# Kernel optimization log

Measured on AMD Instinct MI355X. Metric: run time of the kernel, lower is better.

The kernel has to match this reference:

```python
import jax, jax.numpy as jnp
import numpy as np

INF = 1000000000000.0
B, H, EMB = 64, 512, 512
V = 32000
S_ENC, S_SEQ = 512, 512
ENC2 = 512  # 2 * encoder_hidden_dim
NUM_OOV = 50


def setup_inputs() -> dict:
    key = jax.random.key(0)
    ks = jax.random.split(key, 24)
    s = 0.02
    nrm = lambda k, shp: jax.random.normal(k, shp, jnp.float32) * s
    inp = {}
    inp["input_ids"] = jax.random.randint(ks[0], (B,), 0, V)
    inp["prev_context"] = jax.random.normal(ks[1], (B, H), jnp.float32)
    inp["h0"] = jax.random.normal(ks[2], (1, B, H), jnp.float32)
    inp["c0"] = jax.random.normal(ks[3], (1, B, H), jnp.float32)
    inp["encoder_outputs"] = jax.random.normal(ks[4], (B, S_ENC, H), jnp.float32)
    inp["seqs_encoding"] = jax.random.normal(ks[5], (B, S_SEQ, ENC2), jnp.float32)
    inp["seqs_encoding_mask"] = jax.random.randint(ks[6], (B, S_SEQ), 0, 2).astype(bool)
    ext = jax.random.randint(ks[7], (B, S_SEQ), 0, V + NUM_OOV)
    inp["ext_idx"] = ext.at[0, 0].set(V + NUM_OOV - 1)  # pin max so num_oov=NUM_OOV
    # parameters (torch Linear convention: y = x @ W.T + b)
    inp["embed"] = nrm(ks[8], (V, EMB))
    inp["W_reduce"] = nrm(ks[9], (EMB, EMB + H)); inp["b_reduce"] = jnp.zeros((EMB,), jnp.float32)
    inp["W_key"] = nrm(ks[10], (H, H)); inp["b_key"] = jnp.zeros((H,), jnp.float32)
    inp["W_comb"] = nrm(ks[11], (H, 2 * H)); inp["b_comb"] = jnp.zeros((H,), jnp.float32)
    inp["W_seqkey"] = nrm(ks[12], (H, ENC2))
    inp["W_ih"] = nrm(ks[13], (4 * H, EMB)); inp["W_hh"] = nrm(ks[14], (4 * H, H))
    inp["b_ih"] = jnp.zeros((4 * H,), jnp.float32); inp["b_hh"] = jnp.zeros((4 * H,), jnp.float32)
    inp["W_out"] = nrm(ks[15], (V, H)); inp["b_out"] = jnp.zeros((V,), jnp.float32)
    return inp


def reference(input_ids, prev_context, h0, c0, encoder_outputs, seqs_encoding,
              seqs_encoding_mask, ext_idx, embed, W_reduce, b_reduce, W_key, b_key,
              W_comb, b_comb, W_seqkey, W_ih, W_hh, b_ih, b_hh, W_out, b_out):
    # embed + (dropout is identity at p=0 / eval) + reduce
    embedded = embed[input_ids]                                   # [B, EMB]
    x = jnp.concatenate([embedded, prev_context], axis=1) @ W_reduce.T + b_reduce  # [B, EMB]
    # single-step, single-layer LSTM (PyTorch gate order i, f, g, o)
    h, c = h0[0], c0[0]
    gates = x @ W_ih.T + b_ih + h @ W_hh.T + b_hh                 # [B, 4H]
    i, f, g, o = jnp.split(gates, 4, axis=-1)
    c1 = jax.nn.sigmoid(f) * c + jax.nn.sigmoid(i) * jnp.tanh(g)
    h1 = jax.nn.sigmoid(o) * jnp.tanh(c1)                         # [B, H]
    output = h1
    # masked attention over encoder_outputs
    enc_mask = encoder_outputs.sum(axis=-1) == 0                  # [B, S_enc]
    keys = encoder_outputs @ W_key.T + b_key                      # [B, S_enc, H]
    energies = jnp.einsum('bsh,bh->bs', keys, output)
    energies = jnp.where(enc_mask, 1e-12, energies)
    attn_weights = jax.nn.softmax(energies, axis=-1)
    context = jnp.einsum('bs,bsh->bh', attn_weights, encoder_outputs)  # [B, H]
    combined = jnp.tanh(jnp.concatenate([output, context], axis=1) @ W_comb.T + b_comb)
    logits = combined @ W_out.T + b_out                           # [B, V]
    # masked attention energies over token sequence for the copy mechanism
    seq_keys = jnp.tanh(seqs_encoding @ W_seqkey.T)               # [B, S_seq, H]
    seq_energies = jnp.einsum('bsh,bh->bs', seq_keys, output)
    seq_energies = jnp.where(seqs_encoding_mask, 1e-12, seq_energies)
    # extended vocab + scatter_max pointer-copy
    extended = jnp.concatenate([logits, jnp.zeros((B, NUM_OOV), logits.dtype)], axis=1)  # [B, V+OOV]
    copy = jnp.full_like(extended, -INF)
    copy = copy.at[jnp.arange(B)[:, None], ext_idx].max(seq_energies)
    copy = jnp.where(copy == -INF, 0.0, copy)
    out = extended + copy
    out = jnp.where(out == 0.0, -INF, out)
    out = jax.nn.log_softmax(out, axis=1)
    return (out, context, h1[None], c1[None], attn_weights)
```

## Files before the change

kernel.cpp:

```cpp
#include <hip/hip_runtime.h>
#include <math.h>

#define B_N    64
#define H_N    512
#define V_N    32000
#define S_N    512
#define VEXT   32050
#define INF_F  1000000000000.0f

typedef __attribute__((ext_vector_type(4))) float floatx4;
typedef __attribute__((ext_vector_type(8))) __bf16 bf16x8;

#define OFF_OUT0 0
#define OFF_CTX  (B_N * VEXT)
#define OFF_H1   (OFF_CTX + B_N * H_N)
#define OFF_C1   (OFF_H1 + B_N * H_N)
#define OFF_ATTN (OFF_C1 + B_N * H_N)

#define WS_FLAG   0
#define WS_X      16
#define WS_GATES  (WS_X + B_N * H_N)
#define WS_Q      (WS_GATES + B_N * 4 * H_N)
#define WS_KB     (WS_Q + B_N * H_N)
#define WS_EN     (WS_KB + B_N)
#define WS_COMB   (WS_EN + B_N * S_N)
#define WS_SEQE   (WS_COMB + B_N * H_N)
#define WS_WSKBF  (WS_SEQE + B_N * S_N)
#define WS_LOGITS (WS_WSKBF + (H_N * H_N) / 2)
#define WS_COPY   (WS_LOGITS + B_N * V_N)
#define WS_RMAX   (WS_COPY + B_N * VEXT)
#define WS_RSUM   (WS_RMAX + B_N)

__device__ __forceinline__ float sigm(float x) { return 1.0f / (1.0f + expf(-x)); }

__device__ __forceinline__ unsigned short f2bf(float f) {
    unsigned u = __float_as_uint(f);
    u += 0x7fffu + ((u >> 16) & 1u);
    return (unsigned short)(u >> 16);
}
__device__ __forceinline__ float bf2f(unsigned short h) {
    return __uint_as_float(((unsigned)h) << 16);
}

__device__ __forceinline__ unsigned enc_f(float f) {
    unsigned u = __float_as_uint(f);
    return (u & 0x80000000u) ? ~u : (u | 0x80000000u);
}
__device__ __forceinline__ float dec_f(unsigned e) {
    unsigned u = (e & 0x80000000u) ? (e & 0x7fffffffu) : ~e;
    return __uint_as_float(u);
}

__global__ void kDetect(const unsigned int* __restrict__ m, int* __restrict__ flag) {
    __shared__ int any;
    if (threadIdx.x == 0) any = 0;
    __syncthreads();
    int loc = 0;
    for (int i = threadIdx.x; i < 8192; i += 256) loc |= (m[i] > 1u) ? 1 : 0;
    if (loc) any = 1;
    __syncthreads();
    if (threadIdx.x == 0) *flag = any;
}

__global__ void kConvertW(const float* __restrict__ W, unsigned short* __restrict__ swzh,
                          unsigned short* __restrict__ swzl) {
    const int g = blockIdx.x * 256 + threadIdx.x;
    const int t = g >> 10, kc = (g >> 6) & 15, lane = g & 63;
    const int r = t * 16 + (lane & 15);
    const int k = kc * 32 + (lane >> 4) * 8;
    const float* src = W + (size_t)r * 512 + k;
    ushort4 h0, h1, l0, l1;
    {
        const float4 v0 = *(const float4*)(src);
        const float4 v1 = *(const float4*)(src + 4);
        h0.x = f2bf(v0.x); l0.x = f2bf(v0.x - bf2f(h0.x));
        h0.y = f2bf(v0.y); l0.y = f2bf(v0.y - bf2f(h0.y));
        h0.z = f2bf(v0.z); l0.z = f2bf(v0.z - bf2f(h0.z));
        h0.w = f2bf(v0.w); l0.w = f2bf(v0.w - bf2f(h0.w));
        h1.x = f2bf(v1.x); l1.x = f2bf(v1.x - bf2f(h1.x));
        h1.y = f2bf(v1.y); l1.y = f2bf(v1.y - bf2f(h1.y));
        h1.z = f2bf(v1.z); l1.z = f2bf(v1.z - bf2f(h1.z));
        h1.w = f2bf(v1.w); l1.w = f2bf(v1.w - bf2f(h1.w));
    }
    *(ushort4*)(swzh + (size_t)g * 8) = h0;
    *(ushort4*)(swzh + (size_t)g * 8 + 4) = h1;
    *(ushort4*)(swzl + (size_t)g * 8) = l0;
    *(ushort4*)(swzl + (size_t)g * 8 + 4) = l1;
}

__global__ void kFillCopy(unsigned int* __restrict__ copyenc,
                          unsigned int* __restrict__ rmax, float* __restrict__ rsum) {
    const unsigned NE = enc_f(-INF_F);
    if (blockIdx.x == 0 && threadIdx.x < B_N) {
        rmax[threadIdx.x] = 0u;
        rsum[threadIdx.x] = 0.0f;
    }
    int i0 = (blockIdx.x * 256 + threadIdx.x) * 4;
#pragma unroll
    for (int k = 0; k < 4; k++) {
        int i = i0 + k;
        if (i < B_N * VEXT) copyenc[i] = NE;
    }
}

__global__ __launch_bounds__(256) void kEmbedReduce(
        const int* __restrict__ ids, const float* __restrict__ embed,
        const float* __restrict__ pctx, const float* __restrict__ Wred,
        const float* __restrict__ bred, float* __restrict__ x) {
    __shared__ float xc[1024];
    const int tid = threadIdx.x;
    const int b = blockIdx.x >> 1, half = blockIdx.x & 1;
    const float* er = embed + (size_t)ids[b] * 512;
    xc[tid] = er[tid];               xc[tid + 256] = er[tid + 256];
    xc[512 + tid] = pctx[b * 512 + tid]; xc[512 + tid + 256] = pctx[b * 512 + tid + 256];
    __syncthreads();
    const int j = half * 256 + tid;
    const float4* w4 = (const float4*)(Wred + (size_t)j * 1024);
    const float4* x4 = (const float4*)xc;
    float acc = bred[j];
    for (int k = 0; k < 256; k++) {
        float4 w = w4[k], xv = x4[k];
        acc += w.x * xv.x + w.y * xv.y + w.z * xv.z + w.w * xv.w;
    }
    x[b * 512 + j] = acc;
}

__global__ __launch_bounds__(256) void kGates(
        const float* __restrict__ x, const float* __restrict__ h0,
        const float* __restrict__ Wih, const float* __restrict__ Whh,
        const float* __restrict__ bih, const float* __restrict__ bhh,
        float* __restrict__ gates) {
    __shared__ float xl[512], hl[512];
    const int tid = threadIdx.x;
    const int b = blockIdx.x >> 3, part = blockIdx.x & 7;
    xl[tid] = x[b * 512 + tid];  xl[tid + 256] = x[b * 512 + tid + 256];
    hl[tid] = h0[b * 512 + tid]; hl[tid + 256] = h0[b * 512 + tid + 256];
    __syncthreads();
    const int j = part * 256 + tid;
    const float4* wi4 = (const float4*)(Wih + (size_t)j * 512);
    const float4* wh4 = (const float4*)(Whh + (size_t)j * 512);
    const float4* x4 = (const float4*)xl;
    const float4* h4 = (const float4*)hl;
    float acc = bih[j] + bhh[j];
    for (int k = 0; k < 128; k++) {
        float4 w = wi4[k], xv = x4[k];
        acc += w.x * xv.x + w.y * xv.y + w.z * xv.z + w.w * xv.w;
    }
    for (int k = 0; k < 128; k++) {
        float4 w = wh4[k], hv = h4[k];
        acc += w.x * hv.x + w.y * hv.y + w.z * hv.z + w.w * hv.w;
    }
    gates[(size_t)b * 2048 + j] = acc;
}

__global__ __launch_bounds__(256) void kLstm(
        const float* __restrict__ gates, const float* __restrict__ c0,
        float* __restrict__ h1o, float* __restrict__ c1o) {
    const int idx = blockIdx.x * 256 + threadIdx.x;
    const int b = idx >> 9, j = idx & 511;
    const float gi = gates[(size_t)b * 2048 + j];
    const float gf = gates[(size_t)b * 2048 + 512 + j];
    const float gg = gates[(size_t)b * 2048 + 1024 + j];
    const float go = gates[(size_t)b * 2048 + 1536 + j];
    const float cp = c0[idx];
    const float c1 = sigm(gf) * cp + sigm(gi) * tanhf(gg);
    const float h1 = sigm(go) * tanhf(c1);
    h1o[idx] = h1;
    c1o[idx] = c1;
}

__global__ __launch_bounds__(256) void kQ(
        const float* __restrict__ h1, const float* __restrict__ Wkey,
        const float* __restrict__ bkey, float* __restrict__ q, float* __restrict__ kb) {
    __shared__ float hl[512];
    __shared__ float rd[256];
    const int tid = threadIdx.x;
    const int b = blockIdx.x >> 1, half = blockIdx.x & 1;
    hl[tid] = h1[b * 512 + tid]; hl[tid + 256] = h1[b * 512 + tid + 256];
    __syncthreads();
    const int k = half * 256 + tid;
    float acc = 0.f;
#pragma unroll 4
    for (int h = 0; h < 512; h++) acc += hl[h] * Wkey[(size_t)h * 512 + k];
    q[b * 512 + k] = acc;
    if (half == 0) {
        float p = bkey[tid] * hl[tid] + bkey[tid + 256] * hl[tid + 256];
        rd[tid] = p; __syncthreads();
        for (int st = 128; st > 0; st >>= 1) {
            if (tid < st) rd[tid] += rd[tid + st];
            __syncthreads();
        }
        if (tid == 0) kb[b] = rd[0];
    }
}

__global__ __launch_bounds__(256) void kEnergies(
        const float* __restrict__ enc, const float* __restrict__ q,
        const float* __restrict__ kb, float* __restrict__ energ) {
    __shared__ float ql[512];
    __shared__ float pe[256], ps[256];
    const int tid = threadIdx.x;
    const int b = blockIdx.x >> 2;
    const int sc = (blockIdx.x & 3) * 128;
    ql[tid] = q[b * 512 + tid]; ql[tid + 256] = q[b * 512 + tid + 256];
    __syncthreads();
    const int r = tid & 127, hi = tid >> 7;
    const float4* row4 = (const float4*)(enc + (size_t)(b * 512 + sc + r) * 512 + hi * 256);
    const float4* q4 = (const float4*)(ql + hi * 256);
    float e = 0.f, ssum = 0.f;
#pragma unroll 4
    for (int k = 0; k < 64; k++) {
        float4 ev = row4[k], qv = q4[k];
        e += ev.x * qv.x + ev.y * qv.y + ev.z * qv.z + ev.w * qv.w;
        ssum += ev.x + ev.y + ev.z + ev.w;
    }
    pe[tid] = e; ps[tid] = ssum;
    __syncthreads();
    if (tid < 128) {
        float ee = pe[tid] + pe[tid + 128] + kb[b];
        float sm = ps[tid] + ps[tid + 128];
        if (sm == 0.0f) ee = 1e-12f;
        energ[b * 512 + sc + tid] = ee;
    }
}

__global__ __launch_bounds__(256) void kSoftmax(
        const float* __restrict__ energ, float* __restrict__ attn) {
    __shared__ float el[512];
    __shared__ float rd[256];
    const int tid = threadIdx.x, b = blockIdx.x;
    el[tid] = energ[b * 512 + tid]; el[tid + 256] = energ[b * 512 + tid + 256];
    __syncthreads();
    rd[tid] = fmaxf(el[tid], el[tid + 256]); __syncthreads();
    for (int st = 128; st > 0; st >>= 1) {
        if (tid < st) rd[tid] = fmaxf(rd[tid], rd[tid + st]);
        __syncthreads();
    }
    const float m = rd[0]; __syncthreads();
    float v0 = expf(el[tid] - m), v1 = expf(el[tid + 256] - m);
    rd[tid] = v0 + v1; __syncthreads();
    for (int st = 128; st > 0; st >>= 1) {
        if (tid < st) rd[tid] += rd[tid + st];
        __syncthreads();
    }
    const float inv = 1.0f / rd[0];
    attn[b * 512 + tid] = v0 * inv;
    attn[b * 512 + tid + 256] = v1 * inv;
}

__global__ __launch_bounds__(256) void kContext(
        const float* __restrict__ enc, const float* __restrict__ attn,
        float* __restrict__ ctx) {
    __shared__ float al[64];
    const int tid = threadIdx.x;
    const int b = blockIdx.x >> 3, sc = (blockIdx.x & 7) * 64;
    if (tid < 64) al[tid] = attn[b * 512 + sc + tid];
    __syncthreads();
    float a0 = 0.f, a1 = 0.f;
    for (int s = 0; s < 64; s++) {
        const float* row = enc + (size_t)(b * 512 + sc + s) * 512;
        const float av = al[s];
        a0 += av * row[tid];
        a1 += av * row[tid + 256];
    }
    atomicAdd(&ctx[b * 512 + tid], a0);
    atomicAdd(&ctx[b * 512 + tid + 256], a1);
}

__global__ __launch_bounds__(256) void kCombined(
        const float* __restrict__ h1, const float* __restrict__ ctx,
        const float* __restrict__ Wcomb, const float* __restrict__ bcomb,
        float* __restrict__ comb) {
    __shared__ float hc[1024];
    const int tid = threadIdx.x;
    const int b = blockIdx.x >> 1, half = blockIdx.x & 1;
    hc[tid] = h1[b * 512 + tid];        hc[tid + 256] = h1[b * 512 + tid + 256];
    hc[512 + tid] = ctx[b * 512 + tid]; hc[512 + tid + 256] = ctx[b * 512 + tid + 256];
    __syncthreads();
    const int j = half * 256 + tid;
    const float4* w4 = (const float4*)(Wcomb + (size_t)j * 1024);
    const float4* x4 = (const float4*)hc;
    float acc = bcomb[j];
    for (int k = 0; k < 256; k++) {
        float4 w = w4[k], xv = x4[k];
        acc += w.x * xv.x + w.y * xv.y + w.z * xv.z + w.w * xv.w;
    }
    comb[b * 512 + j] = tanhf(acc);
}

__global__ __launch_bounds__(256) void kLogits(
        const float* __restrict__ comb, const float* __restrict__ Wout,
        const float* __restrict__ bout, float* __restrict__ logits) {
    __shared__ float cl[4][32][64];
    const int tid = threadIdx.x;
    const int vt = tid & 63, kq = tid >> 6;
    const int v = blockIdx.x * 64 + vt;
    float acc[64];
#pragma unroll
    for (int i = 0; i < 64; i++) acc[i] = 0.f;
    for (int kc = 0; kc < 4; kc++) {
        __syncthreads();
        {
            const float4* s4 = (const float4*)(comb + (size_t)vt * 512 + kq * 128 + kc * 32);
#pragma unroll
            for (int qq = 0; qq < 8; qq++) {
                float4 vv = s4[qq];
                cl[kq][qq * 4 + 0][vt] = vv.x; cl[kq][qq * 4 + 1][vt] = vv.y;
                cl[kq][qq * 4 + 2][vt] = vv.z; cl[kq][qq * 4 + 3][vt] = vv.w;
            }
        }
        __syncthreads();
        float wreg[32];
        const float4* w4 = (const float4*)(Wout + (size_t)v * 512 + kq * 128 + kc * 32);
#pragma unroll
        for (int qq = 0; qq < 8; qq++) {
            float4 wv = w4[qq];
            wreg[qq * 4 + 0] = wv.x; wreg[qq * 4 + 1] = wv.y;
            wreg[qq * 4 + 2] = wv.z; wreg[qq * 4 + 3] = wv.w;
        }
#pragma unroll
        for (int kk = 0; kk < 32; kk++) {
            const float wv = wreg[kk];
            const float4* cp = (const float4*)&cl[kq][kk][0];
#pragma unroll
            for (int b4 = 0; b4 < 16; b4++) {
                float4 c4 = cp[b4];
                acc[b4 * 4 + 0] += wv * c4.x; acc[b4 * 4 + 1] += wv * c4.y;
                acc[b4 * 4 + 2] += wv * c4.z; acc[b4 * 4 + 3] += wv * c4.w;
            }
        }
    }
    float* red = &cl[0][0][0];
    __syncthreads();
    if (kq >= 2) {
#pragma unroll
        for (int b = 0; b < 64; b++) red[(kq - 2) * 4096 + vt * 64 + b] = acc[b];
    }
    __syncthreads();
    if (kq < 2) {
#pragma unroll
        for (int b = 0; b < 64; b++) acc[b] += red[kq * 4096 + vt * 64 + b];
    }
    __syncthreads();
    if (kq == 1) {
#pragma unroll
        for (int b = 0; b < 64; b++) red[vt * 64 + b] = acc[b];
    }
    __syncthreads();
    if (kq == 0) {
        const float bo = bout[v];
#pragma unroll
        for (int b = 0; b < 64; b++)
            logits[(size_t)b * 32000 + v] = acc[b] + red[vt * 64 + b] + bo;
    }
}

#define A_STRIDE 520
#define MT 32
__global__ __launch_bounds__(512, 4) void kSeqGemm(
        const float* __restrict__ seqs, const unsigned short* __restrict__ swzh,
        const unsigned short* __restrict__ swzl,
        const float* __restrict__ h1g, float* __restrict__ seq_e) {
    __shared__ unsigned short a_hi[MT * A_STRIDE];
    __shared__ unsigned short a_lo[MT * A_STRIDE];
    __shared__ float h1l[512];
    __shared__ float partf[8][MT];
    const int tid = threadIdx.x;
    const int m0 = blockIdx.x * MT;
    const int b = blockIdx.x >> 4;
    const int w = tid >> 6;
    const int lane = tid & 63;
    const int quad = lane >> 4;
    const int c16 = lane & 15;

    h1l[tid] = h1g[b * 512 + tid];

    {
        const int row = tid >> 4, seg = tid & 15;
        const float* src = seqs + (size_t)(m0 + row) * 512 + seg * 4;
        unsigned short* dh = &a_hi[row * A_STRIDE + seg * 4];
        unsigned short* dl = &a_lo[row * A_STRIDE + seg * 4];
#pragma unroll
        for (int i = 0; i < 8; i++) {
            float4 v = *(const float4*)(src + i * 64);
            ushort4 hv, lv;
            hv.x = f2bf(v.x); lv.x = f2bf(v.x - bf2f(hv.x));
            hv.y = f2bf(v.y); lv.y = f2bf(v.y - bf2f(hv.y));
            hv.z = f2bf(v.z); lv.z = f2bf(v.z - bf2f(hv.z));
            hv.w = f2bf(v.w); lv.w = f2bf(v.w - bf2f(hv.w));
            *(ushort4*)(dh + i * 64) = hv;
            *(ushort4*)(dl + i * 64) = lv;
        }
    }
    __syncthreads();

    floatx4 acc[2][4];
    const floatx4 zf = {0.f, 0.f, 0.f, 0.f};
#pragma unroll
    for (int i = 0; i < 2; i++)
#pragma unroll
        for (int j = 0; j < 4; j++) acc[i][j] = zf;

    const size_t boff = (size_t)((w * 4) * 16) * 512 + (size_t)lane * 8;
    const unsigned short* bh = swzh + boff;
    const unsigned short* bl = swzl + boff;
#pragma unroll 2
    for (int kc = 0; kc < 16; kc++) {
        bf16x8 ah[2], al[2], bhf[4], blf[4];
#pragma unroll
        for (int nt = 0; nt < 4; nt++) {
            bhf[nt] = *(const bf16x8*)(bh + (size_t)(nt * 16 + kc) * 512);
            blf[nt] = *(const bf16x8*)(bl + (size_t)(nt * 16 + kc) * 512);
        }
#pragma unroll
        for (int ms = 0; ms < 2; ms++) {
            ah[ms] = *(const bf16x8*)&a_hi[(ms * 16 + c16) * A_STRIDE + kc * 32 + quad * 8];
            al[ms] = *(const bf16x8*)&a_lo[(ms * 16 + c16) * A_STRIDE + kc * 32 + quad * 8];
        }
#pragma unroll
        for (int ms = 0; ms < 2; ms++)
#pragma unroll
            for (int nt = 0; nt < 4; nt++) {
                acc[ms][nt] = __builtin_amdgcn_mfma_f32_16x16x32_bf16(
                    ah[ms], bhf[nt], acc[ms][nt], 0, 0, 0);
                acc[ms][nt] = __builtin_amdgcn_mfma_f32_16x16x32_bf16(
                    al[ms], bhf[nt], acc[ms][nt], 0, 0, 0);
                acc[ms][nt] = __builtin_amdgcn_mfma_f32_16x16x32_bf16(
                    ah[ms], blf[nt], acc[ms][nt], 0, 0, 0);
            }
    }

    float psum[8];
#pragma unroll
    for (int i = 0; i < 8; i++) psum[i] = 0.f;
#pragma unroll
    for (int ms = 0; ms < 2; ms++)
#pragma unroll
        for (int nt = 0; nt < 4; nt++) {
            const float hv = h1l[w * 64 + nt * 16 + c16];
#pragma unroll
            for (int r = 0; r < 4; r++)
                psum[ms * 4 + r] += tanhf(acc[ms][nt][r]) * hv;
        }
#pragma unroll
    for (int d = 1; d < 16; d <<= 1)
#pragma unroll
        for (int i = 0; i < 8; i++) psum[i] += __shfl_xor(psum[i], d);
    if (c16 == 0) {
#pragma unroll
        for (int ms = 0; ms < 2; ms++)
#pragma unroll
            for (int r = 0; r < 4; r++)
                partf[w][ms * 16 + quad * 4 + r] = psum[ms * 4 + r];
    }
    __syncthreads();
    if (tid < MT) {
        float s = 0.f;
#pragma unroll
        for (int ww = 0; ww < 8; ww++) s += partf[ww][tid];
        seq_e[m0 + tid] = s;
    }
}

__global__ __launch_bounds__(512) void kScatter(
        const float* __restrict__ seq_e, const void* __restrict__ mask,
        const int* __restrict__ extix, const int* __restrict__ flag,
        unsigned int* __restrict__ copyenc) {
    const int tid = threadIdx.x, b = blockIdx.x;
    float e = seq_e[b * 512 + tid];
    bool mk;
    if (*flag) mk = ((const unsigned char*)mask)[b * 512 + tid] != 0;
    else       mk = ((const int*)mask)[b * 512 + tid] != 0;
    if (mk) e = 1e-12f;
    const int idx = extix[b * 512 + tid];
    atomicMax(&copyenc[(size_t)b * VEXT + idx], enc_f(e));
}

__global__ __launch_bounds__(256) void kFinal1(
        const float* __restrict__ logits, const unsigned int* __restrict__ copyenc,
        float* __restrict__ out0, unsigned int* __restrict__ rmax) {
    __shared__ float rd[4];
    const int tid = threadIdx.x;
    const int b = blockIdx.x >> 4, chunk = blockIdx.x & 15;
    const int base = chunk * 2048 + tid;
    const float* lrow = logits + (size_t)b * 32000;
    const unsigned int* crow = copyenc + (size_t)b * VEXT;
    float* orow = out0 + (size_t)b * VEXT;
    float lm = -3.0e38f;
#pragma unroll
    for (int k = 0; k < 8; k++) {
        const int j = base + k * 256;
        if (j < VEXT) {
            float ext = (j < 32000) ? lrow[j] : 0.0f;
            float cv = dec_f(crow[j]);
            if (cv == -INF_F) cv = 0.0f;
            float o = ext + cv;
            if (o == 0.0f) o = -INF_F;
            orow[j] = o;
            lm = fmaxf(lm, o);
        }
    }
#pragma unroll
    for (int d = 1; d < 64; d <<= 1) lm = fmaxf(lm, __shfl_xor(lm, d));
    if ((tid & 63) == 0) rd[tid >> 6] = lm;
    __syncthreads();
    if (tid == 0) {
        float m = fmaxf(fmaxf(rd[0], rd[1]), fmaxf(rd[2], rd[3]));
        atomicMax(&rmax[b], enc_f(m));
    }
}

__global__ __launch_bounds__(256) void kFinal2(
        const float* __restrict__ out0, const unsigned int* __restrict__ rmax,
        float* __restrict__ rsum) {
    __shared__ float rd[4];
    const int tid = threadIdx.x;
    const int b = blockIdx.x >> 4, chunk = blockIdx.x & 15;
    const int base = chunk * 2048 + tid;
    const float* orow = out0 + (size_t)b * VEXT;
    const float m = dec_f(rmax[b]);
    float s = 0.f;
#pragma unroll
    for (int k = 0; k < 8; k++) {
        const int j = base + k * 256;
        if (j < VEXT) s += expf(orow[j] - m);
    }
#pragma unroll
    for (int d = 1; d < 64; d <<= 1) s += __shfl_xor(s, d);
    if ((tid & 63) == 0) rd[tid >> 6] = s;
    __syncthreads();
    if (tid == 0) atomicAdd(&rsum[b], rd[0] + rd[1] + rd[2] + rd[3]);
}

__global__ __launch_bounds__(256) void kFinal3(
        float* __restrict__ out0, const unsigned int* __restrict__ rmax,
        const float* __restrict__ rsum) {
    const int tid = threadIdx.x;
    const int b = blockIdx.x >> 4, chunk = blockIdx.x & 15;
    const int base = chunk * 2048 + tid;
    float* orow = out0 + (size_t)b * VEXT;
    const float lse = dec_f(rmax[b]) + logf(rsum[b]);
#pragma unroll
    for (int k = 0; k < 8; k++) {
        const int j = base + k * 256;
        if (j < VEXT) orow[j] -= lse;
    }
}

extern "C" void kernel_launch(void* const* d_in, const int* in_sizes, int n_in,
                              void* d_out, int out_size, void* d_ws, size_t ws_size,
                              hipStream_t stream) {
    const int*   ids   = (const int*)d_in[0];
    const float* pctx  = (const float*)d_in[1];
    const float* h0    = (const float*)d_in[2];
    const float* c0    = (const float*)d_in[3];
    const float* enc   = (const float*)d_in[4];
    const float* seqs  = (const float*)d_in[5];
    const void*  mask  = d_in[6];
    const int*   extix = (const int*)d_in[7];
    const float* embed = (const float*)d_in[8];
    const float* Wred  = (const float*)d_in[9];
    const float* bred  = (const float*)d_in[10];
    const float* Wkey  = (const float*)d_in[11];
    const float* bkey  = (const float*)d_in[12];
    const float* Wcomb = (const float*)d_in[13];
    const float* bcomb = (const float*)d_in[14];
    const float* Wseqk = (const float*)d_in[15];
    const float* Wih   = (const float*)d_in[16];
    const float* Whh   = (const float*)d_in[17];
    const float* bih   = (const float*)d_in[18];
    const float* bhh   = (const float*)d_in[19];
    const float* Wout  = (const float*)d_in[20];
    const float* bout  = (const float*)d_in[21];
    (void)in_sizes; (void)n_in; (void)out_size; (void)ws_size;

    float* out = (float*)d_out;
    float* ws = (float*)d_ws;
    int* flag = (int*)ws;
    float* xws = ws + WS_X;
    float* gatesws = ws + WS_GATES;
    float* qws = ws + WS_Q;
    float* kbws = ws + WS_KB;
    float* enws = ws + WS_EN;
    float* combws = ws + WS_COMB;
    float* seqews = ws + WS_SEQE;
    unsigned short* wskh = (unsigned short*)(ws + WS_WSKBF);
    float* logitsws = ws + WS_LOGITS;
    unsigned short* wskl = (unsigned short*)(ws + WS_LOGITS);
    unsigned int* copyenc = (unsigned int*)(ws + WS_COPY);
    unsigned int* rmax = (unsigned int*)(ws + WS_RMAX);
    float* rsum = ws + WS_RSUM;

    kDetect<<<1, 256, 0, stream>>>((const unsigned int*)mask, flag);
    kConvertW<<<128, 256, 0, stream>>>(Wseqk, wskh, wskl);
    kFillCopy<<<2004, 256, 0, stream>>>(copyenc, rmax, rsum);
    kEmbedReduce<<<128, 256, 0, stream>>>(ids, embed, pctx, Wred, bred, xws);
    kGates<<<512, 256, 0, stream>>>(xws, h0, Wih, Whh, bih, bhh, gatesws);
    kLstm<<<128, 256, 0, stream>>>(gatesws, c0, out + OFF_H1, out + OFF_C1);
    kSeqGemm<<<1024, 512, 0, stream>>>(seqs, wskh, wskl, out + OFF_H1, seqews);
    kScatter<<<64, 512, 0, stream>>>(seqews, mask, extix, flag, copyenc);
    kQ<<<128, 256, 0, stream>>>(out + OFF_H1, Wkey, bkey, qws, kbws);
    kEnergies<<<256, 256, 0, stream>>>(enc, qws, kbws, enws);
    kSoftmax<<<64, 256, 0, stream>>>(enws, out + OFF_ATTN);
    hipMemsetAsync(out + OFF_CTX, 0, (size_t)B_N * H_N * sizeof(float), stream);
    kContext<<<512, 256, 0, stream>>>(enc, out + OFF_ATTN, out + OFF_CTX);
    kCombined<<<128, 256, 0, stream>>>(out + OFF_H1, out + OFF_CTX, Wcomb, bcomb, combws);
    kLogits<<<500, 256, 0, stream>>>(combws, Wout, bout, logitsws);
    kFinal1<<<1024, 256, 0, stream>>>(logitsws, copyenc, out + OFF_OUT0, rmax);
    kFinal2<<<1024, 256, 0, stream>>>(out + OFF_OUT0, rmax, rsum);
    kFinal3<<<1024, 256, 0, stream>>>(out + OFF_OUT0, rmax, rsum);
}
```

Measured before the change: 592.3 us.

## Enlarge seq-key GEMM tile to 128 rows with K-chunking and fuse scatter-max

The seq-key GEMM block tile grows from 32 to 128 rows. The A operand is staged through shared memory in four K-chunks of 128, so each W_seqkey fragment loaded from global memory is reused across 8 M-subtiles instead of 2. This cuts B-operand traffic and the block count from 1024 to 256, at the cost of many more accumulator registers (occupancy hint drops to 2) and extra barriers per chunk. The separate scatter kernel is folded into the GEMM epilogue, which removes one launch and the seq_e round trip through global memory.

```diff
diff --git a/kernel.cpp b/kernel.cpp
--- a/kernel.cpp
+++ b/kernel.cpp
@@ -355,19 +355,19 @@
     }
 }
 
-#define A_STRIDE 520
-#define MT 32
-__global__ __launch_bounds__(512, 4) void kSeqGemm(
+#define ACH 136
+__global__ __launch_bounds__(512, 2) void kSeqGemm(
         const float* __restrict__ seqs, const unsigned short* __restrict__ swzh,
-        const unsigned short* __restrict__ swzl,
-        const float* __restrict__ h1g, float* __restrict__ seq_e) {
-    __shared__ unsigned short a_hi[MT * A_STRIDE];
-    __shared__ unsigned short a_lo[MT * A_STRIDE];
+        const unsigned short* __restrict__ swzl, const float* __restrict__ h1g,
+        const void* __restrict__ mask, const int* __restrict__ extix,
+        const int* __restrict__ flag, unsigned int* __restrict__ copyenc) {
+    __shared__ unsigned short a_hi[128 * ACH];
+    __shared__ unsigned short a_lo[128 * ACH];
     __shared__ float h1l[512];
-    __shared__ float partf[8][MT];
-    const int tid = threadIdx.x;
-    const int m0 = blockIdx.x * MT;
-    const int b = blockIdx.x >> 4;
+    __shared__ float partf[8][128];
+    const int tid = threadIdx.x;
+    const int m0 = blockIdx.x * 128;
+    const int b = blockIdx.x >> 2;
     const int w = tid >> 6;
     const int lane = tid & 63;
     const int quad = lane >> 4;
@@ -375,66 +375,69 @@
 
     h1l[tid] = h1g[b * 512 + tid];
 
-    {
-        const int row = tid >> 4, seg = tid & 15;
-        const float* src = seqs + (size_t)(m0 + row) * 512 + seg * 4;
-        unsigned short* dh = &a_hi[row * A_STRIDE + seg * 4];
-        unsigned short* dl = &a_lo[row * A_STRIDE + seg * 4];
-#pragma unroll
-        for (int i = 0; i < 8; i++) {
-            float4 v = *(const float4*)(src + i * 64);
-            ushort4 hv, lv;
-            hv.x = f2bf(v.x); lv.x = f2bf(v.x - bf2f(hv.x));
-            hv.y = f2bf(v.y); lv.y = f2bf(v.y - bf2f(hv.y));
-            hv.z = f2bf(v.z); lv.z = f2bf(v.z - bf2f(hv.z));
-            hv.w = f2bf(v.w); lv.w = f2bf(v.w - bf2f(hv.w));
-            *(ushort4*)(dh + i * 64) = hv;
-            *(ushort4*)(dl + i * 64) = lv;
-        }
-    }
-    __syncthreads();
-
-    floatx4 acc[2][4];
+    floatx4 acc[8][4];
     const floatx4 zf = {0.f, 0.f, 0.f, 0.f};
 #pragma unroll
-    for (int i = 0; i < 2; i++)
+    for (int i = 0; i < 8; i++)
 #pragma unroll
         for (int j = 0; j < 4; j++) acc[i][j] = zf;
 
-    const size_t boff = (size_t)((w * 4) * 16) * 512 + (size_t)lane * 8;
+    const size_t boff = (size_t)(w * 64) * 512 + (size_t)lane * 8;
     const unsigned short* bh = swzh + boff;
     const unsigned short* bl = swzl + boff;
-#pragma unroll 2
-    for (int kc = 0; kc < 16; kc++) {
-        bf16x8 ah[2], al[2], bhf[4], blf[4];
-#pragma unroll
-        for (int nt = 0; nt < 4; nt++) {
-            bhf[nt] = *(const bf16x8*)(bh + (size_t)(nt * 16 + kc) * 512);
-            blf[nt] = *(const bf16x8*)(bl + (size_t)(nt * 16 + kc) * 512);
-        }
-#pragma unroll
-        for (int ms = 0; ms < 2; ms++) {
-            ah[ms] = *(const bf16x8*)&a_hi[(ms * 16 + c16) * A_STRIDE + kc * 32 + quad * 8];
-            al[ms] = *(const bf16x8*)&a_lo[(ms * 16 + c16) * A_STRIDE + kc * 32 + quad * 8];
-        }
-#pragma unroll
-        for (int ms = 0; ms < 2; ms++)
+
+    const int srow = tid >> 2, sq = tid & 3;
+
+    for (int c = 0; c < 4; c++) {
+        __syncthreads();
+        {
+            const float* src = seqs + (size_t)(m0 + srow) * 512 + c * 128 + sq * 32;
+            unsigned short* dh = &a_hi[srow * ACH + sq * 32];
+            unsigned short* dl = &a_lo[srow * ACH + sq * 32];
+#pragma unroll
+            for (int i = 0; i < 8; i++) {
+                float4 v = *(const float4*)(src + i * 4);
+                ushort4 hv, lv;
+                hv.x = f2bf(v.x); lv.x = f2bf(v.x - bf2f(hv.x));
+                hv.y = f2bf(v.y); lv.y = f2bf(v.y - bf2f(hv.y));
+                hv.z = f2bf(v.z); lv.z = f2bf(v.z - bf2f(hv.z));
+                hv.w = f2bf(v.w); lv.w = f2bf(v.w - bf2f(hv.w));
+                *(ushort4*)(dh + i * 4) = hv;
+                *(ushort4*)(dl + i * 4) = lv;
+            }
+        }
+        __syncthreads();
+#pragma unroll
+        for (int kcl = 0; kcl < 4; kcl++) {
+            const int kc = c * 4 + kcl;
+            bf16x8 bhf[4], blf[4];
 #pragma unroll
             for (int nt = 0; nt < 4; nt++) {
-                acc[ms][nt] = __builtin_amdgcn_mfma_f32_16x16x32_bf16(
-                    ah[ms], bhf[nt], acc[ms][nt], 0, 0, 0);
-                acc[ms][nt] = __builtin_amdgcn_mfma_f32_16x16x32_bf16(
-                    al[ms], bhf[nt], acc[ms][nt], 0, 0, 0);
-                acc[ms][nt] = __builtin_amdgcn_mfma_f32_16x16x32_bf16(
-                    ah[ms], blf[nt], acc[ms][nt], 0, 0, 0);
+                bhf[nt] = *(const bf16x8*)(bh + (size_t)(nt * 16 + kc) * 512);
+                blf[nt] = *(const bf16x8*)(bl + (size_t)(nt * 16 + kc) * 512);
             }
-    }
-
-    float psum[8];
-#pragma unroll
-    for (int i = 0; i < 8; i++) psum[i] = 0.f;
-#pragma unroll
-    for (int ms = 0; ms < 2; ms++)
+#pragma unroll
+            for (int ms = 0; ms < 8; ms++) {
+                bf16x8 ah = *(const bf16x8*)&a_hi[(ms * 16 + c16) * ACH + kcl * 32 + quad * 8];
+                bf16x8 al = *(const bf16x8*)&a_lo[(ms * 16 + c16) * ACH + kcl * 32 + quad * 8];
+#pragma unroll
+                for (int nt = 0; nt < 4; nt++) {
+                    acc[ms][nt] = __builtin_amdgcn_mfma_f32_16x16x32_bf16(
+                        ah, bhf[nt], acc[ms][nt], 0, 0, 0);
+                    acc[ms][nt] = __builtin_amdgcn_mfma_f32_16x16x32_bf16(
+                        al, bhf[nt], acc[ms][nt], 0, 0, 0);
+                    acc[ms][nt] = __builtin_amdgcn_mfma_f32_16x16x32_bf16(
+                        ah, blf[nt], acc[ms][nt], 0, 0, 0);
+                }
+            }
+        }
+    }
+
+    float psum[32];
+#pragma unroll
+    for (int i = 0; i < 32; i++) psum[i] = 0.f;
+#pragma unroll
+    for (int ms = 0; ms < 8; ms++)
 #pragma unroll
         for (int nt = 0; nt < 4; nt++) {
             const float hv = h1l[w * 64 + nt * 16 + c16];
@@ -445,35 +448,27 @@
 #pragma unroll
     for (int d = 1; d < 16; d <<= 1)
 #pragma unroll
-        for (int i = 0; i < 8; i++) psum[i] += __shfl_xor(psum[i], d);
+        for (int i = 0; i < 32; i++) psum[i] += __shfl_xor(psum[i], d);
     if (c16 == 0) {
 #pragma unroll
-        for (int ms = 0; ms < 2; ms++)
+        for (int ms = 0; ms < 8; ms++)
 #pragma unroll
             for (int r = 0; r < 4; r++)
                 partf[w][ms * 16 + quad * 4 + r] = psum[ms * 4 + r];
     }
     __syncthreads();
-    if (tid < MT) {
+    if (tid < 128) {
         float s = 0.f;
 #pragma unroll
         for (int ww = 0; ww < 8; ww++) s += partf[ww][tid];
-        seq_e[m0 + tid] = s;
-    }
-}
-
-__global__ __launch_bounds__(512) void kScatter(
-        const float* __restrict__ seq_e, const void* __restrict__ mask,
-        const int* __restrict__ extix, const int* __restrict__ flag,
-        unsigned int* __restrict__ copyenc) {
-    const int tid = threadIdx.x, b = blockIdx.x;
-    float e = seq_e[b * 512 + tid];
-    bool mk;
-    if (*flag) mk = ((const unsigned char*)mask)[b * 512 + tid] != 0;
-    else       mk = ((const int*)mask)[b * 512 + tid] != 0;
-    if (mk) e = 1e-12f;
-    const int idx = extix[b * 512 + tid];
-    atomicMax(&copyenc[(size_t)b * VEXT + idx], enc_f(e));
+        const int m = m0 + tid;
+        bool mk;
+        if (*flag) mk = ((const unsigned char*)mask)[m] != 0;
+        else       mk = ((const int*)mask)[m] != 0;
+        if (mk) s = 1e-12f;
+        const int idx = extix[m];
+        atomicMax(&copyenc[(size_t)b * VEXT + idx], enc_f(s));
+    }
 }
 
 __global__ __launch_bounds__(256) void kFinal1(
@@ -583,7 +578,6 @@
     float* kbws = ws + WS_KB;
     float* enws = ws + WS_EN;
     float* combws = ws + WS_COMB;
-    float* seqews = ws + WS_SEQE;
     unsigned short* wskh = (unsigned short*)(ws + WS_WSKBF);
     float* logitsws = ws + WS_LOGITS;
     unsigned short* wskl = (unsigned short*)(ws + WS_LOGITS);
@@ -597,8 +591,8 @@
     kEmbedReduce<<<128, 256, 0, stream>>>(ids, embed, pctx, Wred, bred, xws);
     kGates<<<512, 256, 0, stream>>>(xws, h0, Wih, Whh, bih, bhh, gatesws);
     kLstm<<<128, 256, 0, stream>>>(gatesws, c0, out + OFF_H1, out + OFF_C1);
-    kSeqGemm<<<1024, 512, 0, stream>>>(seqs, wskh, wskl, out + OFF_H1, seqews);
-    kScatter<<<64, 512, 0, stream>>>(seqews, mask, extix, flag, copyenc);
+    kSeqGemm<<<256, 512, 0, stream>>>(seqs, wskh, wskl, out + OFF_H1,
+                                      mask, extix, flag, copyenc);
     kQ<<<128, 256, 0, stream>>>(out + OFF_H1, Wkey, bkey, qws, kbws);
     kEnergies<<<256, 256, 0, stream>>>(enc, qws, kbws, enws);
     kSoftmax<<<64, 256, 0, stream>>>(enws, out + OFF_ATTN);
```

Result: no change. 597.6 us (+0.9%).
